# Optimization experiments

Measured on AMD Instinct MI355X. Metric: run time of the kernel, lower is better.

## Reference

```python
import jax, jax.numpy as jnp
import numpy as np

BATCH = 32768
HIDDEN = 512
OUT = 2
FUTURE_STEPS = 60


def _lstm_cell(x, h, c, w_ih, w_hh, b_ih, b_hh):
    # PyTorch gate order: i, f, g, o
    g = x @ w_ih.T + h @ w_hh.T + b_ih + b_hh
    i, f, gg, o = jnp.split(g, 4, axis=-1)
    c_new = jax.nn.sigmoid(f) * c + jax.nn.sigmoid(i) * jnp.tanh(gg)
    h_new = jax.nn.sigmoid(o) * jnp.tanh(c_new)
    return h_new, c_new


def setup_inputs() -> dict:
    key = jax.random.key(0)
    ks = jax.random.split(key, 16)
    s = 0.05
    inp = {
        "h": jax.random.normal(ks[0], (BATCH, HIDDEN), jnp.float32),
        "w_init_h": jax.random.normal(ks[1], (HIDDEN, HIDDEN), jnp.float32) * s,
        "b_init_h": jax.random.normal(ks[2], (HIDDEN,), jnp.float32) * s,
        "w_init_c": jax.random.normal(ks[3], (HIDDEN, HIDDEN), jnp.float32) * s,
        "b_init_c": jax.random.normal(ks[4], (HIDDEN,), jnp.float32) * s,
        "w_ih0": jax.random.normal(ks[5], (4 * HIDDEN, OUT), jnp.float32) * s,
        "w_hh0": jax.random.normal(ks[6], (4 * HIDDEN, HIDDEN), jnp.float32) * s,
        "b_ih0": jax.random.normal(ks[7], (4 * HIDDEN,), jnp.float32) * s,
        "b_hh0": jax.random.normal(ks[8], (4 * HIDDEN,), jnp.float32) * s,
        "w_ih1": jax.random.normal(ks[9], (4 * HIDDEN, HIDDEN), jnp.float32) * s,
        "w_hh1": jax.random.normal(ks[10], (4 * HIDDEN, HIDDEN), jnp.float32) * s,
        "b_ih1": jax.random.normal(ks[11], (4 * HIDDEN,), jnp.float32) * s,
        "b_hh1": jax.random.normal(ks[12], (4 * HIDDEN,), jnp.float32) * s,
        "w_out": jax.random.normal(ks[13], (OUT, HIDDEN), jnp.float32) * s,
        "b_out": jax.random.normal(ks[14], (OUT,), jnp.float32) * s,
    }
    return inp


def reference(h, w_init_h, b_init_h, w_init_c, b_init_c,
              w_ih0, w_hh0, b_ih0, b_hh0,
              w_ih1, w_hh1, b_ih1, b_hh1,
              w_out, b_out):
    batch = h.shape[0]
    # same initial (h, c) replicated to both LSTM layers (repeat(2,1,1))
    h0 = h @ w_init_h.T + b_init_h
    c0 = h @ w_init_c.T + b_init_c
    x0 = jnp.zeros((batch, OUT), h.dtype)

    def step(carry, _):
        x, h1, c1, h2, c2 = carry
        h1, c1 = _lstm_cell(x, h1, c1, w_ih0, w_hh0, b_ih0, b_hh0)
        h2, c2 = _lstm_cell(h1, h2, c2, w_ih1, w_hh1, b_ih1, b_hh1)
        pred = h2 @ w_out.T + b_out  # [batch, OUT]
        return (pred, h1, c1, h2, c2), pred

    _, preds = jax.lax.scan(step, (x0, h0, c0, h0, c0), None, length=FUTURE_STEPS)
    return jnp.transpose(preds, (1, 0, 2))  # [batch, future_steps, OUT]
```

## Files before the change

kernel.cpp:

```cpp
#include <hip/hip_runtime.h>

#define HID    512
#define TPB    512
#define NSTEP  60
#define BMI    64

using f32x4 = __attribute__((ext_vector_type(4))) float;
using s16x8 = __attribute__((ext_vector_type(8))) short;

__device__ __forceinline__ unsigned short f2bf(float f) {
    unsigned u = __builtin_bit_cast(unsigned, f);
    u += 0x7fffu + ((u >> 16) & 1u);
    return (unsigned short)(u >> 16);
}
__device__ __forceinline__ float bf2f(unsigned u) {
    return __builtin_bit_cast(float, u << 16);
}
__device__ __forceinline__ float sigm(float x) { return 1.0f / (1.0f + __expf(-x)); }
__device__ __forceinline__ float tanh_(float x) { return 1.0f - 2.0f / (__expf(2.0f * x) + 1.0f); }

__device__ __forceinline__ f32x4 deperm(f32x4 q, int lgr) {
    f32x4 p;
    if (lgr == 0)      { p[0]=q[0]; p[1]=q[1]; p[2]=q[2]; p[3]=q[3]; }
    else if (lgr == 1) { p[0]=q[1]; p[1]=q[0]; p[2]=q[3]; p[3]=q[2]; }
    else if (lgr == 2) { p[0]=q[2]; p[1]=q[3]; p[2]=q[0]; p[3]=q[1]; }
    else               { p[0]=q[3]; p[1]=q[2]; p[2]=q[1]; p[3]=q[0]; }
    return p;
}

__global__ void pack_kernel(const float* __restrict__ w_hh0, const float* __restrict__ w_ih1,
                            const float* __restrict__ w_hh1, const float* __restrict__ w_init_h,
                            const float* __restrict__ w_init_c,
                            const float* __restrict__ b_ih0, const float* __restrict__ b_hh0,
                            const float* __restrict__ b_ih1, const float* __restrict__ b_hh1,
                            unsigned short* __restrict__ PW1, unsigned short* __restrict__ PW2,
                            unsigned short* __restrict__ PI,
                            float* __restrict__ b1, float* __restrict__ b2)
{
    int idx = blockIdx.x * 256 + threadIdx.x;
    if (idx < 1048576) {
        int el = idx & 511, fr = idx >> 9;
        int ks = fr & 15, ct = (fr >> 4) & 7, s = fr >> 7;
        int lane = el >> 3, e = el & 7;
        int cl = ct * 16 + (lane & 15);
        int gcol = (cl >> 5) * 512 + s * 32 + (cl & 31);
        int k = ks * 32 + (lane >> 4) * 8 + e;
        PW1[idx] = f2bf(w_hh0[gcol * 512 + k]);
        return;
    }
    int i2 = idx - 1048576;
    if (i2 >= 0 && i2 < 2097152) {
        int el = i2 & 511, fr = i2 >> 9;
        int ks = fr & 31, ct = (fr >> 5) & 7, s = fr >> 8;
        int lane = el >> 3, e = el & 7;
        int cl = ct * 16 + (lane & 15);
        int gcol = (cl >> 5) * 512 + s * 32 + (cl & 31);
        int kk = (ks & 15) * 32 + (lane >> 4) * 8 + e;
        float v = (ks < 16) ? w_ih1[gcol * 512 + kk] : w_hh1[gcol * 512 + kk];
        PW2[i2] = f2bf(v);
        return;
    }
    int i3 = idx - (1048576 + 2097152);
    if (i3 >= 0 && i3 < 524288) {
        int el = i3 & 511, fr = i3 >> 9;
        int ks = fr & 15, tile = fr >> 4;
        int s = tile >> 5, c = tile & 31;
        int lane = el >> 3, e = el & 7;
        int n = c * 16 + (lane & 15);
        int k = ks * 32 + (lane >> 4) * 8 + e;
        float v = s ? w_init_c[n * 512 + k] : w_init_h[n * 512 + k];
        PI[i3] = f2bf(v);
        return;
    }
    int i4 = idx - (1048576 + 2097152 + 524288);
    if (i4 >= 0 && i4 < 2048) b1[i4] = b_ih0[i4] + b_hh0[i4];
    else if (i4 >= 2048 && i4 < 4096) b2[i4 - 2048] = b_ih1[i4 - 2048] + b_hh1[i4 - 2048];
}

__global__ __launch_bounds__(TPB, 2) void init_kernel(
    const float* __restrict__ hin, const unsigned short* __restrict__ PI,
    const float* __restrict__ b_init_h, const float* __restrict__ b_init_c,
    unsigned short* __restrict__ h1s, unsigned short* __restrict__ h2s,
    unsigned short* __restrict__ c1s, unsigned short* __restrict__ c2s)
{
    __shared__ unsigned short bufA[BMI * HID];
    const int tid = threadIdx.x, lane = tid & 63, wave = tid >> 6;
    const int m0 = blockIdx.x * BMI;
    const int l15 = lane & 15, lg = lane >> 4;
    const int swz = (lane & 7) << 4;

    for (int j = 0; j < 16; ++j) {
        int e = tid * 4 + j * 2048;
        int row = e >> 9, col = e & 511;
        float4 v = *(const float4*)(hin + (size_t)(m0 + row) * HID + col);
        ushort4 w;
        w.x = f2bf(v.x); w.y = f2bf(v.y); w.z = f2bf(v.z); w.w = f2bf(v.w);
        int L = (row * 1024 + col * 2) ^ ((row & 7) << 4);
        *(ushort4*)((char*)bufA + L) = w;
    }
    __syncthreads();

    #pragma unroll 1
    for (int cc = 0; cc < 4; ++cc) {
        int c = wave * 4 + cc;
        int nc = c * 16 + l15;
        f32x4 acc[4][2];
        #pragma unroll
        for (int rt = 0; rt < 4; ++rt)
            #pragma unroll
            for (int s = 0; s < 2; ++s)
                #pragma unroll
                for (int r = 0; r < 4; ++r) acc[rt][s][r] = 0.0f;

        #pragma unroll
        for (int ks = 0; ks < 16; ++ks) {
            s16x8 a[4];
            #pragma unroll
            for (int rt = 0; rt < 4; ++rt) {
                int ao = (rt * 16 + l15) * 1024 + ((ks * 64 + lg * 16) ^ swz);
                a[rt] = *(const s16x8*)((const char*)bufA + ao);
            }
            #pragma unroll
            for (int s = 0; s < 2; ++s) {
                s16x8 b = ((const s16x8*)PI)[((s * 32 + c) * 16 + ks) * 64 + lane];
                #pragma unroll
                for (int rt = 0; rt < 4; ++rt)
                    acc[rt][s] = __builtin_amdgcn_mfma_f32_16x16x32_bf16(a[rt], b, acc[rt][s], 0, 0, 0);
            }
        }
        float bh = b_init_h[nc], bc = b_init_c[nc];
        #pragma unroll
        for (int rt = 0; rt < 4; ++rt)
            #pragma unroll
            for (int r = 0; r < 4; ++r) {
                int m = m0 + rt * 16 + lg * 4 + r;
                float hv = acc[rt][0][r] + bh;
                float cv = acc[rt][1][r] + bc;
                unsigned short hb = f2bf(hv);
                size_t o = (size_t)m * HID + nc;
                h1s[o] = hb; h2s[o] = hb;
                c1s[o] = f2bf(cv); c2s[o] = f2bf(cv);
            }
    }
}

__global__ __launch_bounds__(TPB, 2) void l1_kernel(
    const unsigned short* __restrict__ h1R, unsigned short* __restrict__ h1W,
    unsigned short* __restrict__ c1s, const float* __restrict__ pp,
    float* __restrict__ outp, const unsigned short* __restrict__ PW1,
    const float* __restrict__ b1, const float* __restrict__ w_ih0,
    const float* __restrict__ b_out, int t)
{
    __shared__ __align__(16) unsigned short Ab[16384];
    __shared__ __align__(16) float gl[2][2][2048];
    __shared__ __align__(16) float xls[5120];

    const int tid = threadIdx.x, lane = tid & 63, w = tid >> 6;
    const int b = blockIdx.x;
    const int g = 2 * (b & 7) + (b >> 7);
    const int s = (b >> 3) & 15;
    const int m0 = g * 2048;
    const int l15 = lane & 15, lg = lane >> 4;
    const int cg = w & 1, kh = (w >> 1) & 1, rha = w >> 2;

    s16x8 bw[4][8];
    #pragma unroll
    for (int j = 0; j < 4; ++j)
        #pragma unroll
        for (int ksl = 0; ksl < 8; ++ksl)
            bw[j][ksl] = ((const s16x8*)PW1)[(((s * 8 + cg * 4 + j) * 16) + kh * 8 + ksl) * 64 + lane];

    const int erow = tid >> 4, ejp = tid & 15;
    const int lgr = w & 3;
    float b1v[8], wiA[8], wiB[8];
    #pragma unroll
    for (int q = 0; q < 8; ++q) {
        int dj = q & 1, gq = q >> 1;
        int gcol = gq * 512 + s * 32 + ejp * 2 + dj;
        b1v[q] = b1[gcol];
        wiA[q] = w_ih0[gcol * 2 + 0];
        wiB[q] = w_ih0[gcol * 2 + 1];
    }
    float bo0 = b_out[0], bo1 = b_out[1];

    if (t == 0) {
        #pragma unroll
        for (int i = 0; i < 8; ++i) xls[tid * 8 + i] = 0.0f;
    } else {
        f32x4 s0 = {0.f,0.f,0.f,0.f}, s1 = {0.f,0.f,0.f,0.f};
        #pragma unroll 1
        for (int ss = 0; ss < 16; ++ss) {
            const float* p = pp + (((size_t)(g * 16 + ss)) << 12) + tid * 8;
            s0 += *(const f32x4*)p;
            s1 += *(const f32x4*)(p + 4);
        }
        s0[0] += bo0; s0[1] += bo1; s0[2] += bo0; s0[3] += bo1;
        s1[0] += bo0; s1[1] += bo1; s1[2] += bo0; s1[3] += bo1;
        *(f32x4*)(xls + tid * 8) = s0;
        *(f32x4*)(xls + tid * 8 + 4) = s1;
        if (s == 0) {
            float* ob = outp + (size_t)(m0 + tid * 4) * (2 * NSTEP) + (t - 1) * 2;
            *(float2*)(ob)                 = make_float2(s0[0], s0[1]);
            *(float2*)(ob + 2 * NSTEP)     = make_float2(s0[2], s0[3]);
            *(float2*)(ob + 4 * NSTEP)     = make_float2(s1[0], s1[1]);
            *(float2*)(ob + 6 * NSTEP)     = make_float2(s1[2], s1[3]);
        }
    }

    const int st_l15 = tid & 15, st_lg = (tid >> 4) & 3, st_rh = (tid >> 6) & 1, st_kq = tid >> 7;
    const int st_grow = st_rh * 16 + st_l15;

    uint4 nv[4];
    #pragma unroll
    for (int p = 0; p < 4; ++p) {
        int ks = p * 4 + st_kq;
        nv[p] = *(const uint4*)(h1R + (size_t)(m0 + st_grow) * HID + ks * 32 + st_lg * 8);
    }
    #pragma unroll
    for (int p = 0; p < 4; ++p)
        *(uint4*)((char*)Ab + p * 8192 + tid * 16) = nv[p];

    #pragma unroll 1
    for (int ch = 0; ch < 64; ++ch) {
        __syncthreads();

        if (ch < 63) {
            #pragma unroll
            for (int p = 0; p < 4; ++p) {
                int ks = p * 4 + st_kq;
                nv[p] = *(const uint4*)(h1R + (size_t)(m0 + (ch + 1) * 32 + st_grow) * HID + ks * 32 + st_lg * 8);
            }
        }

        f32x4 acc[4];
        #pragma unroll
        for (int j = 0; j < 4; ++j) { acc[j][0]=0.f; acc[j][1]=0.f; acc[j][2]=0.f; acc[j][3]=0.f; }
        #pragma unroll
        for (int ksl = 0; ksl < 8; ++ksl) {
            int ks = kh * 8 + ksl;
            s16x8 a = *(const s16x8*)((const char*)Ab + ks * 2048 + rha * 1024 + lane * 16);
            #pragma unroll
            for (int j = 0; j < 4; ++j)
                acc[j] = __builtin_amdgcn_mfma_f32_16x16x32_bf16(a, bw[j][ksl], acc[j], 0, 0, 0);
        }
        #pragma unroll
        for (int j = 0; j < 4; ++j) {
            int col = (cg * 4 + j) * 16 + l15;
            int u = col & 31, gate = col >> 5;
            float* dst = &gl[kh][u & 1][(u >> 1) * 4 + (gate ^ lg)];
            #pragma unroll
            for (int r = 0; r < 4; ++r)
                dst[(rha * 16 + lg * 4 + r) * 64] = acc[j][r];
        }
        __syncthreads();

        if (ch < 63) {
            #pragma unroll
            for (int p = 0; p < 4; ++p)
                *(uint4*)((char*)Ab + p * 8192 + tid * 16) = nv[p];
        }

        {
            int grow = ch * 32 + erow;
            int m = m0 + grow;
            float x0 = xls[grow * 2 + 0], x1 = xls[grow * 2 + 1];
            int gbase = erow * 64 + ejp * 4;
            f32x4 qa = *(const f32x4*)&gl[0][0][gbase];
            qa += *(const f32x4*)&gl[1][0][gbase];
            f32x4 qb = *(const f32x4*)&gl[0][1][gbase];
            qb += *(const f32x4*)&gl[1][1][gbase];
            qa = deperm(qa, lgr); qb = deperm(qb, lgr);

            int cix = m * HID + s * 32 + ejp * 2;
            unsigned cp = *(const unsigned*)(c1s + cix);
            float cold0 = bf2f(cp & 0xffffu), cold1 = bf2f(cp >> 16);
            float i0 = sigm(qa[0] + b1v[0] + x0 * wiA[0] + x1 * wiB[0]);
            float f0 = sigm(qa[1] + b1v[2] + x0 * wiA[2] + x1 * wiB[2]);
            float g0 = tanh_(qa[2] + b1v[4] + x0 * wiA[4] + x1 * wiB[4]);
            float o0 = sigm(qa[3] + b1v[6] + x0 * wiA[6] + x1 * wiB[6]);
            float cn0 = f0 * cold0 + i0 * g0;
            float hn0 = o0 * tanh_(cn0);
            float i1 = sigm(qb[0] + b1v[1] + x0 * wiA[1] + x1 * wiB[1]);
            float f1 = sigm(qb[1] + b1v[3] + x0 * wiA[3] + x1 * wiB[3]);
            float g1 = tanh_(qb[2] + b1v[5] + x0 * wiA[5] + x1 * wiB[5]);
            float o1 = sigm(qb[3] + b1v[7] + x0 * wiA[7] + x1 * wiB[7]);
            float cn1 = f1 * cold1 + i1 * g1;
            float hn1 = o1 * tanh_(cn1);
            __builtin_nontemporal_store((unsigned)f2bf(cn0) | ((unsigned)f2bf(cn1) << 16),
                                        (unsigned*)(c1s + cix));
            __builtin_nontemporal_store((unsigned)f2bf(hn0) | ((unsigned)f2bf(hn1) << 16),
                                        (unsigned*)(h1W + cix));
        }
    }
}

__global__ __launch_bounds__(TPB, 2) void l2_kernel(
    const unsigned short* __restrict__ h1C, const unsigned short* __restrict__ h2R,
    unsigned short* __restrict__ h2W, unsigned short* __restrict__ c2s,
    float* __restrict__ pp,
    const unsigned short* __restrict__ PW2, const float* __restrict__ b2,
    const float* __restrict__ w_out)
{
    __shared__ __align__(16) unsigned short Ab[32768];
    __shared__ __align__(16) float gl[2][2][2304];

    const int tid = threadIdx.x, lane = tid & 63, w = tid >> 6;
    const int b = blockIdx.x;
    const int g = 2 * (b & 7) + (b >> 7);
    const int s = (b >> 3) & 15;
    const int m0 = g * 2048;
    const int l15 = lane & 15, lg = lane >> 4;
    const int cg = w & 1, kq = w >> 1;
    const int copy = kq >> 1, adder = ((kq & 1) == 0);

    s16x8 bw[4][8];
    #pragma unroll
    for (int j = 0; j < 4; ++j)
        #pragma unroll
        for (int ksl = 0; ksl < 8; ++ksl)
            bw[j][ksl] = ((const s16x8*)PW2)[(((s * 8 + cg * 4 + j) * 32) + kq * 8 + ksl) * 64 + lane];

    const int erow = tid >> 4, ejp = tid & 15;
    const int lgr = w & 3;
    float b2v[8];
    #pragma unroll
    for (int q = 0; q < 8; ++q) {
        int dj = q & 1, gq = q >> 1;
        b2v[q] = b2[gq * 512 + s * 32 + ejp * 2 + dj];
    }
    float woA0 = w_out[s * 32 + ejp * 2], woA1 = w_out[s * 32 + ejp * 2 + 1];
    float woB0 = w_out[512 + s * 32 + ejp * 2], woB1 = w_out[512 + s * 32 + ejp * 2 + 1];

    const int st_l15 = tid & 15, st_lg = (tid >> 4) & 3, st_rh = (tid >> 6) & 1, st_kq = tid >> 7;
    const int st_grow = st_rh * 16 + st_l15;

    uint4 nv[8];
    #pragma unroll
    for (int p = 0; p < 8; ++p) {
        int ks = p * 4 + st_kq;
        const unsigned short* src = (ks < 16) ? h1C : h2R;
        int kel = (ks < 16) ? ks : (ks - 16);
        nv[p] = *(const uint4*)(src + (size_t)(m0 + st_grow) * HID + kel * 32 + st_lg * 8);
    }
    #pragma unroll
    for (int p = 0; p < 8; ++p)
        *(uint4*)((char*)Ab + p * 8192 + tid * 16) = nv[p];

    #pragma unroll 1
    for (int ch = 0; ch < 64; ++ch) {
        __syncthreads();

        if (ch < 63) {
            #pragma unroll
            for (int p = 0; p < 8; ++p) {
                int ks = p * 4 + st_kq;
                const unsigned short* src = (ks < 16) ? h1C : h2R;
                int kel = (ks < 16) ? ks : (ks - 16);
                nv[p] = *(const uint4*)(src + (size_t)(m0 + (ch + 1) * 32 + st_grow) * HID + kel * 32 + st_lg * 8);
            }
        }

        f32x4 acc[2][4];
        #pragma unroll
        for (int rh = 0; rh < 2; ++rh)
            #pragma unroll
            for (int j = 0; j < 4; ++j) { acc[rh][j][0]=0.f; acc[rh][j][1]=0.f; acc[rh][j][2]=0.f; acc[rh][j][3]=0.f; }
        #pragma unroll
        for (int ksl = 0; ksl < 8; ++ksl) {
            int ks = kq * 8 + ksl;
            s16x8 a0 = *(const s16x8*)((const char*)Ab + ks * 2048 + lane * 16);
            s16x8 a1 = *(const s16x8*)((const char*)Ab + ks * 2048 + 1024 + lane * 16);
            #pragma unroll
            for (int j = 0; j < 4; ++j) {
                acc[0][j] = __builtin_amdgcn_mfma_f32_16x16x32_bf16(a0, bw[j][ksl], acc[0][j], 0, 0, 0);
                acc[1][j] = __builtin_amdgcn_mfma_f32_16x16x32_bf16(a1, bw[j][ksl], acc[1][j], 0, 0, 0);
            }
        }

        if (!adder) {
            #pragma unroll
            for (int j = 0; j < 4; ++j) {
                int col = (cg * 4 + j) * 16 + l15;
                int u = col & 31, gate = col >> 5;
                float* dst = &gl[copy][u & 1][(u >> 1) * 4 + (gate ^ lg)];
                #pragma unroll
                for (int rh = 0; rh < 2; ++rh)
                    #pragma unroll
                    for (int r = 0; r < 4; ++r)
                        dst[(rh * 16 + lg * 4 + r) * 64] = acc[rh][j][r];
            }
        }
        __syncthreads();
        if (adder) {
            #pragma unroll
            for (int j = 0; j < 4; ++j) {
                int col = (cg * 4 + j) * 16 + l15;
                int u = col & 31, gate = col >> 5;
                float* dst = &gl[copy][u & 1][(u >> 1) * 4 + (gate ^ lg)];
                #pragma unroll
                for (int rh = 0; rh < 2; ++rh)
                    #pragma unroll
                    for (int r = 0; r < 4; ++r)
                        dst[(rh * 16 + lg * 4 + r) * 64] += acc[rh][j][r];
            }
        }
        __syncthreads();

        if (ch < 63) {
            #pragma unroll
            for (int p = 0; p < 8; ++p)
                *(uint4*)((char*)Ab + p * 8192 + tid * 16) = nv[p];
        }

        {
            int m = m0 + ch * 32 + erow;
            int gbase = erow * 64 + ejp * 4;
            f32x4 qa = *(const f32x4*)&gl[0][0][gbase];
            qa += *(const f32x4*)&gl[1][0][gbase];
            f32x4 qb = *(const f32x4*)&gl[0][1][gbase];
            qb += *(const f32x4*)&gl[1][1][gbase];
            qa = deperm(qa, lgr); qb = deperm(qb, lgr);

            int cix = m * HID + s * 32 + ejp * 2;
            unsigned cp = *(const unsigned*)(c2s + cix);
            float cold0 = bf2f(cp & 0xffffu), cold1 = bf2f(cp >> 16);
            float i0 = sigm(qa[0] + b2v[0]);
            float f0 = sigm(qa[1] + b2v[2]);
            float g0 = tanh_(qa[2] + b2v[4]);
            float o0 = sigm(qa[3] + b2v[6]);
            float cn0 = f0 * cold0 + i0 * g0;
            float hn0 = o0 * tanh_(cn0);
            float i1 = sigm(qb[0] + b2v[1]);
            float f1 = sigm(qb[1] + b2v[3]);
            float g1 = tanh_(qb[2] + b2v[5]);
            float o1 = sigm(qb[3] + b2v[7]);
            float cn1 = f1 * cold1 + i1 * g1;
            float hn1 = o1 * tanh_(cn1);
            __builtin_nontemporal_store((unsigned)f2bf(cn0) | ((unsigned)f2bf(cn1) << 16),
                                        (unsigned*)(c2s + cix));
            __builtin_nontemporal_store((unsigned)f2bf(hn0) | ((unsigned)f2bf(hn1) << 16),
                                        (unsigned*)(h2W + cix));

            float p0 = hn0 * woA0 + hn1 * woA1;
            float p1 = hn0 * woB0 + hn1 * woB1;
            #pragma unroll
            for (int d = 1; d < 16; d <<= 1) {
                p0 += __shfl_xor(p0, d, 16);
                p1 += __shfl_xor(p1, d, 16);
            }
            if (ejp == 0)
                *(float2*)(pp + (((size_t)(g * 16 + s)) << 12) + (size_t)(ch * 32 + erow) * 2)
                    = make_float2(p0, p1);
        }
    }
}

__global__ void tail_kernel(const float* __restrict__ pp, const float* __restrict__ b_out,
                            float* __restrict__ outp)
{
    int i = blockIdx.x * 256 + threadIdx.x;
    if (i < 65536) {
        int m = i >> 1, j = i & 1;
        int g = m >> 11;
        int idx = (m & 2047) * 2 + j;
        float sum = b_out[j];
        #pragma unroll 1
        for (int s = 0; s < 16; ++s)
            sum += pp[(((size_t)(g * 16 + s)) << 12) + idx];
        outp[(size_t)m * (2 * NSTEP) + (NSTEP - 1) * 2 + j] = sum;
    }
}

extern "C" void kernel_launch(void* const* d_in, const int* in_sizes, int n_in,
                              void* d_out, int out_size, void* d_ws, size_t ws_size,
                              hipStream_t stream)
{
    (void)in_sizes; (void)n_in; (void)out_size; (void)ws_size;
    const float* h        = (const float*)d_in[0];
    const float* w_init_h = (const float*)d_in[1];
    const float* b_init_h = (const float*)d_in[2];
    const float* w_init_c = (const float*)d_in[3];
    const float* b_init_c = (const float*)d_in[4];
    const float* w_ih0    = (const float*)d_in[5];
    const float* w_hh0    = (const float*)d_in[6];
    const float* b_ih0    = (const float*)d_in[7];
    const float* b_hh0    = (const float*)d_in[8];
    const float* w_ih1    = (const float*)d_in[9];
    const float* w_hh1    = (const float*)d_in[10];
    const float* b_ih1    = (const float*)d_in[11];
    const float* b_hh1    = (const float*)d_in[12];
    const float* w_out    = (const float*)d_in[13];
    const float* b_out    = (const float*)d_in[14];
    float* out = (float*)d_out;

    char* ws = (char*)d_ws;
    unsigned short* h1s[2] = { (unsigned short*)(ws + 0),
                               (unsigned short*)(ws + 33554432) };
    unsigned short* h2s[2] = { (unsigned short*)(ws + 67108864),
                               (unsigned short*)(ws + 100663296) };
    unsigned short* c1s = (unsigned short*)(ws + 134217728);
    unsigned short* c2s = (unsigned short*)(ws + 167772160);
    float* pp           = (float*)(ws + 201326592);
    unsigned short* PW1 = (unsigned short*)(ws + 205520896);
    unsigned short* PW2 = (unsigned short*)(ws + 207618048);
    unsigned short* PI  = (unsigned short*)(ws + 211812352);
    float* b1 = (float*)(ws + 212860928);
    float* b2 = (float*)(ws + 212869120);

    pack_kernel<<<14352, 256, 0, stream>>>(w_hh0, w_ih1, w_hh1, w_init_h, w_init_c,
                                           b_ih0, b_hh0, b_ih1, b_hh1, PW1, PW2, PI, b1, b2);
    init_kernel<<<32768 / BMI, TPB, 0, stream>>>(h, PI, b_init_h, b_init_c,
                                                 h1s[1], h2s[1], c1s, c2s);
    for (int t = 0; t < NSTEP; ++t) {
        const unsigned short* h1R = h1s[(t + 1) & 1];
        unsigned short* h1W = h1s[t & 1];
        const unsigned short* h2R = h2s[(t + 1) & 1];
        unsigned short* h2W = h2s[t & 1];
        l1_kernel<<<256, TPB, 0, stream>>>(h1R, h1W, c1s, pp, out, PW1, b1, w_ih0, b_out, t);
        l2_kernel<<<256, TPB, 0, stream>>>(h1W, h2R, h2W, c2s, pp, PW2, b2, w_out);
    }
    tail_kernel<<<256, 256, 0, stream>>>(pp, b_out, out);
}
```

Baseline: 41.11 ms.

## Reorder packed weight columns and restructure LSTM step kernels' pipeline and gate reduction

```diff
diff --git a/kernel.cpp b/kernel.cpp
--- a/kernel.cpp
+++ b/kernel.cpp
@@ -18,15 +18,6 @@
 }
 __device__ __forceinline__ float sigm(float x) { return 1.0f / (1.0f + __expf(-x)); }
 __device__ __forceinline__ float tanh_(float x) { return 1.0f - 2.0f / (__expf(2.0f * x) + 1.0f); }
-
-__device__ __forceinline__ f32x4 deperm(f32x4 q, int lgr) {
-    f32x4 p;
-    if (lgr == 0)      { p[0]=q[0]; p[1]=q[1]; p[2]=q[2]; p[3]=q[3]; }
-    else if (lgr == 1) { p[0]=q[1]; p[1]=q[0]; p[2]=q[3]; p[3]=q[2]; }
-    else if (lgr == 2) { p[0]=q[2]; p[1]=q[3]; p[2]=q[0]; p[3]=q[1]; }
-    else               { p[0]=q[3]; p[1]=q[2]; p[2]=q[1]; p[3]=q[0]; }
-    return p;
-}
 
 __global__ void pack_kernel(const float* __restrict__ w_hh0, const float* __restrict__ w_ih1,
                             const float* __restrict__ w_hh1, const float* __restrict__ w_init_h,
@@ -42,8 +33,8 @@
         int el = idx & 511, fr = idx >> 9;
         int ks = fr & 15, ct = (fr >> 4) & 7, s = fr >> 7;
         int lane = el >> 3, e = el & 7;
-        int cl = ct * 16 + (lane & 15);
-        int gcol = (cl >> 5) * 512 + s * 32 + (cl & 31);
+        int l15 = lane & 15;
+        int gcol = (l15 & 3) * 512 + s * 32 + ct * 4 + (l15 >> 2);
         int k = ks * 32 + (lane >> 4) * 8 + e;
         PW1[idx] = f2bf(w_hh0[gcol * 512 + k]);
         return;
@@ -53,8 +44,8 @@
         int el = i2 & 511, fr = i2 >> 9;
         int ks = fr & 31, ct = (fr >> 5) & 7, s = fr >> 8;
         int lane = el >> 3, e = el & 7;
-        int cl = ct * 16 + (lane & 15);
-        int gcol = (cl >> 5) * 512 + s * 32 + (cl & 31);
+        int l15 = lane & 15;
+        int gcol = (l15 & 3) * 512 + s * 32 + ct * 4 + (l15 >> 2);
         int kk = (ks & 15) * 32 + (lane >> 4) * 8 + e;
         float v = (ks < 16) ? w_ih1[gcol * 512 + kk] : w_hh1[gcol * 512 + kk];
         PW2[i2] = f2bf(v);
@@ -152,8 +143,8 @@
     const float* __restrict__ b_out, int t)
 {
     __shared__ __align__(16) unsigned short Ab[16384];
-    __shared__ __align__(16) float gl[2][2][2048];
-    __shared__ __align__(16) float xls[5120];
+    __shared__ __align__(16) float glf[2 * 4224];
+    __shared__ __align__(16) float xls[4096];
 
     const int tid = threadIdx.x, lane = tid & 63, w = tid >> 6;
     const int b = blockIdx.x;
@@ -161,17 +152,16 @@
     const int s = (b >> 3) & 15;
     const int m0 = g * 2048;
     const int l15 = lane & 15, lg = lane >> 4;
-    const int cg = w & 1, kh = (w >> 1) & 1, rha = w >> 2;
-
-    s16x8 bw[4][8];
-    #pragma unroll
-    for (int j = 0; j < 4; ++j)
+    const int cg = w >> 1, kh = w & 1;
+
+    s16x8 bw[2][8];
+    #pragma unroll
+    for (int j = 0; j < 2; ++j)
         #pragma unroll
         for (int ksl = 0; ksl < 8; ++ksl)
-            bw[j][ksl] = ((const s16x8*)PW1)[(((s * 8 + cg * 4 + j) * 16) + kh * 8 + ksl) * 64 + lane];
+            bw[j][ksl] = ((const s16x8*)PW1)[(((s * 8 + cg * 2 + j) * 16) + kh * 8 + ksl) * 64 + lane];
 
     const int erow = tid >> 4, ejp = tid & 15;
-    const int lgr = w & 3;
     float b1v[8], wiA[8], wiB[8];
     #pragma unroll
     for (int q = 0; q < 8; ++q) {
@@ -200,10 +190,10 @@
         *(f32x4*)(xls + tid * 8 + 4) = s1;
         if (s == 0) {
             float* ob = outp + (size_t)(m0 + tid * 4) * (2 * NSTEP) + (t - 1) * 2;
-            *(float2*)(ob)                 = make_float2(s0[0], s0[1]);
-            *(float2*)(ob + 2 * NSTEP)     = make_float2(s0[2], s0[3]);
-            *(float2*)(ob + 4 * NSTEP)     = make_float2(s1[0], s1[1]);
-            *(float2*)(ob + 6 * NSTEP)     = make_float2(s1[2], s1[3]);
+            *(float2*)(ob)             = make_float2(s0[0], s0[1]);
+            *(float2*)(ob + 2 * NSTEP) = make_float2(s0[2], s0[3]);
+            *(float2*)(ob + 4 * NSTEP) = make_float2(s1[0], s1[1]);
+            *(float2*)(ob + 6 * NSTEP) = make_float2(s1[2], s1[3]);
         }
     }
 
@@ -214,66 +204,73 @@
     #pragma unroll
     for (int p = 0; p < 4; ++p) {
         int ks = p * 4 + st_kq;
-        nv[p] = *(const uint4*)(h1R + (size_t)(m0 + st_grow) * HID + ks * 32 + st_lg * 8);
-    }
-    #pragma unroll
-    for (int p = 0; p < 4; ++p)
-        *(uint4*)((char*)Ab + p * 8192 + tid * 16) = nv[p];
+        uint4 v = *(const uint4*)(h1R + (size_t)(m0 + st_grow) * HID + ks * 32 + st_lg * 8);
+        *(uint4*)((char*)Ab + p * 8192 + tid * 16) = v;
+    }
+    #pragma unroll
+    for (int p = 0; p < 4; ++p) {
+        int ks = p * 4 + st_kq;
+        nv[p] = *(const uint4*)(h1R + (size_t)(m0 + 32 + st_grow) * HID + ks * 32 + st_lg * 8);
+    }
+    unsigned cpr = *(const unsigned*)(c1s + (size_t)(m0 + erow) * HID + s * 32 + ejp * 2);
+    __syncthreads();
 
     #pragma unroll 1
     for (int ch = 0; ch < 64; ++ch) {
+        f32x4 acc[2][2];
+        #pragma unroll
+        for (int j = 0; j < 2; ++j)
+            #pragma unroll
+            for (int rh = 0; rh < 2; ++rh) { acc[j][rh][0]=0.f; acc[j][rh][1]=0.f; acc[j][rh][2]=0.f; acc[j][rh][3]=0.f; }
+        #pragma unroll
+        for (int ksl = 0; ksl < 8; ++ksl) {
+            int ks = kh * 8 + ksl;
+            s16x8 a0 = *(const s16x8*)((const char*)Ab + ks * 2048 + lane * 16);
+            s16x8 a1 = *(const s16x8*)((const char*)Ab + ks * 2048 + 1024 + lane * 16);
+            #pragma unroll
+            for (int j = 0; j < 2; ++j) {
+                acc[j][0] = __builtin_amdgcn_mfma_f32_16x16x32_bf16(a0, bw[j][ksl], acc[j][0], 0, 0, 0);
+                acc[j][1] = __builtin_amdgcn_mfma_f32_16x16x32_bf16(a1, bw[j][ksl], acc[j][1], 0, 0, 0);
+            }
+        }
+        #pragma unroll
+        for (int j = 0; j < 2; ++j) {
+            int col = (cg * 2 + j) * 16 + l15;
+            #pragma unroll
+            for (int rh = 0; rh < 2; ++rh)
+                #pragma unroll
+                for (int r = 0; r < 4; ++r)
+                    glf[kh * 4224 + (rh * 16 + lg * 4 + r) * 132 + col] = acc[j][rh][r];
+        }
         __syncthreads();
 
         if (ch < 63) {
+            #pragma unroll
+            for (int p = 0; p < 4; ++p)
+                *(uint4*)((char*)Ab + p * 8192 + tid * 16) = nv[p];
+        }
+        if (ch < 62) {
             #pragma unroll
             for (int p = 0; p < 4; ++p) {
                 int ks = p * 4 + st_kq;
-                nv[p] = *(const uint4*)(h1R + (size_t)(m0 + (ch + 1) * 32 + st_grow) * HID + ks * 32 + st_lg * 8);
-            }
-        }
-
-        f32x4 acc[4];
-        #pragma unroll
-        for (int j = 0; j < 4; ++j) { acc[j][0]=0.f; acc[j][1]=0.f; acc[j][2]=0.f; acc[j][3]=0.f; }
-        #pragma unroll
-        for (int ksl = 0; ksl < 8; ++ksl) {
-            int ks = kh * 8 + ksl;
-            s16x8 a = *(const s16x8*)((const char*)Ab + ks * 2048 + rha * 1024 + lane * 16);
-            #pragma unroll
-            for (int j = 0; j < 4; ++j)
-                acc[j] = __builtin_amdgcn_mfma_f32_16x16x32_bf16(a, bw[j][ksl], acc[j], 0, 0, 0);
-        }
-        #pragma unroll
-        for (int j = 0; j < 4; ++j) {
-            int col = (cg * 4 + j) * 16 + l15;
-            int u = col & 31, gate = col >> 5;
-            float* dst = &gl[kh][u & 1][(u >> 1) * 4 + (gate ^ lg)];
-            #pragma unroll
-            for (int r = 0; r < 4; ++r)
-                dst[(rha * 16 + lg * 4 + r) * 64] = acc[j][r];
-        }
-        __syncthreads();
-
-        if (ch < 63) {
-            #pragma unroll
-            for (int p = 0; p < 4; ++p)
-                *(uint4*)((char*)Ab + p * 8192 + tid * 16) = nv[p];
-        }
+                nv[p] = *(const uint4*)(h1R + (size_t)(m0 + (ch + 2) * 32 + st_grow) * HID + ks * 32 + st_lg * 8);
+            }
+        }
+        unsigned cnx = 0;
+        if (ch < 63)
+            cnx = *(const unsigned*)(c1s + (size_t)(m0 + (ch + 1) * 32 + erow) * HID + s * 32 + ejp * 2);
 
         {
             int grow = ch * 32 + erow;
             int m = m0 + grow;
             float x0 = xls[grow * 2 + 0], x1 = xls[grow * 2 + 1];
-            int gbase = erow * 64 + ejp * 4;
-            f32x4 qa = *(const f32x4*)&gl[0][0][gbase];
-            qa += *(const f32x4*)&gl[1][0][gbase];
-            f32x4 qb = *(const f32x4*)&gl[0][1][gbase];
-            qb += *(const f32x4*)&gl[1][1][gbase];
-            qa = deperm(qa, lgr); qb = deperm(qb, lgr);
-
-            int cix = m * HID + s * 32 + ejp * 2;
-            unsigned cp = *(const unsigned*)(c1s + cix);
-            float cold0 = bf2f(cp & 0xffffu), cold1 = bf2f(cp >> 16);
+            int gbase = erow * 132 + ejp * 8;
+            f32x4 qa = *(const f32x4*)&glf[gbase];
+            qa += *(const f32x4*)&glf[4224 + gbase];
+            f32x4 qb = *(const f32x4*)&glf[gbase + 4];
+            qb += *(const f32x4*)&glf[4224 + gbase + 4];
+
+            float cold0 = bf2f(cpr & 0xffffu), cold1 = bf2f(cpr >> 16);
             float i0 = sigm(qa[0] + b1v[0] + x0 * wiA[0] + x1 * wiB[0]);
             float f0 = sigm(qa[1] + b1v[2] + x0 * wiA[2] + x1 * wiB[2]);
             float g0 = tanh_(qa[2] + b1v[4] + x0 * wiA[4] + x1 * wiB[4]);
@@ -286,11 +283,12 @@
             float o1 = sigm(qb[3] + b1v[7] + x0 * wiA[7] + x1 * wiB[7]);
             float cn1 = f1 * cold1 + i1 * g1;
             float hn1 = o1 * tanh_(cn1);
-            __builtin_nontemporal_store((unsigned)f2bf(cn0) | ((unsigned)f2bf(cn1) << 16),
-                                        (unsigned*)(c1s + cix));
-            __builtin_nontemporal_store((unsigned)f2bf(hn0) | ((unsigned)f2bf(hn1) << 16),
-                                        (unsigned*)(h1W + cix));
-        }
+            size_t cix = (size_t)m * HID + s * 32 + ejp * 2;
+            *(unsigned*)(c1s + cix) = (unsigned)f2bf(cn0) | ((unsigned)f2bf(cn1) << 16);
+            *(unsigned*)(h1W + cix) = (unsigned)f2bf(hn0) | ((unsigned)f2bf(hn1) << 16);
+        }
+        cpr = cnx;
+        __syncthreads();
     }
 }
 
@@ -302,7 +300,7 @@
     const float* __restrict__ w_out)
 {
     __shared__ __align__(16) unsigned short Ab[32768];
-    __shared__ __align__(16) float gl[2][2][2304];
+    __shared__ __align__(16) float glf[2 * 4224];
 
     const int tid = threadIdx.x, lane = tid & 63, w = tid >> 6;
     const int b = blockIdx.x;
@@ -310,18 +308,16 @@
     const int s = (b >> 3) & 15;
     const int m0 = g * 2048;
     const int l15 = lane & 15, lg = lane >> 4;
-    const int cg = w & 1, kq = w >> 1;
-    const int copy = kq >> 1, adder = ((kq & 1) == 0);
-
-    s16x8 bw[4][8];
-    #pragma unroll
-    for (int j = 0; j < 4; ++j)
-        #pragma unroll
-        for (int ksl = 0; ksl < 8; ++ksl)
-            bw[j][ksl] = ((const s16x8*)PW2)[(((s * 8 + cg * 4 + j) * 32) + kq * 8 + ksl) * 64 + lane];
+    const int cg = w >> 1, kh = w & 1;
+
+    s16x8 bw[2][16];
+    #pragma unroll
+    for (int j = 0; j < 2; ++j)
+        #pragma unroll
+        for (int ksl = 0; ksl < 16; ++ksl)
+            bw[j][ksl] = ((const s16x8*)PW2)[(((s * 8 + cg * 2 + j) * 32) + kh * 16 + ksl) * 64 + lane];
 
     const int erow = tid >> 4, ejp = tid & 15;
-    const int lgr = w & 3;
     float b2v[8];
     #pragma unroll
     for (int q = 0; q < 8; ++q) {
@@ -340,90 +336,76 @@
         int ks = p * 4 + st_kq;
         const unsigned short* src = (ks < 16) ? h1C : h2R;
         int kel = (ks < 16) ? ks : (ks - 16);
-        nv[p] = *(const uint4*)(src + (size_t)(m0 + st_grow) * HID + kel * 32 + st_lg * 8);
-    }
-    #pragma unroll
-    for (int p = 0; p < 8; ++p)
-        *(uint4*)((char*)Ab + p * 8192 + tid * 16) = nv[p];
+        uint4 v = *(const uint4*)(src + (size_t)(m0 + st_grow) * HID + kel * 32 + st_lg * 8);
+        *(uint4*)((char*)Ab + p * 8192 + tid * 16) = v;
+    }
+    #pragma unroll
+    for (int p = 0; p < 8; ++p) {
+        int ks = p * 4 + st_kq;
+        const unsigned short* src = (ks < 16) ? h1C : h2R;
+        int kel = (ks < 16) ? ks : (ks - 16);
+        nv[p] = *(const uint4*)(src + (size_t)(m0 + 32 + st_grow) * HID + kel * 32 + st_lg * 8);
+    }
+    unsigned cpr = *(const unsigned*)(c2s + (size_t)(m0 + erow) * HID + s * 32 + ejp * 2);
+    __syncthreads();
 
     #pragma unroll 1
     for (int ch = 0; ch < 64; ++ch) {
+        f32x4 acc[2][2];
+        #pragma unroll
+        for (int j = 0; j < 2; ++j)
+            #pragma unroll
+            for (int rh = 0; rh < 2; ++rh) { acc[j][rh][0]=0.f; acc[j][rh][1]=0.f; acc[j][rh][2]=0.f; acc[j][rh][3]=0.f; }
+        #pragma unroll
+        for (int ksl = 0; ksl < 16; ++ksl) {
+            int ks = kh * 16 + ksl;
+            s16x8 a0 = *(const s16x8*)((const char*)Ab + ks * 2048 + lane * 16);
+            s16x8 a1 = *(const s16x8*)((const char*)Ab + ks * 2048 + 1024 + lane * 16);
+            #pragma unroll
+            for (int j = 0; j < 2; ++j) {
+                acc[j][0] = __builtin_amdgcn_mfma_f32_16x16x32_bf16(a0, bw[j][ksl], acc[j][0], 0, 0, 0);
+                acc[j][1] = __builtin_amdgcn_mfma_f32_16x16x32_bf16(a1, bw[j][ksl], acc[j][1], 0, 0, 0);
+            }
+        }
+        #pragma unroll
+        for (int j = 0; j < 2; ++j) {
+            int col = (cg * 2 + j) * 16 + l15;
+            #pragma unroll
+            for (int rh = 0; rh < 2; ++rh)
+                #pragma unroll
+                for (int r = 0; r < 4; ++r)
+                    glf[kh * 4224 + (rh * 16 + lg * 4 + r) * 132 + col] = acc[j][rh][r];
+        }
         __syncthreads();
 
         if (ch < 63) {
+            #pragma unroll
+            for (int p = 0; p < 8; ++p)
+                *(uint4*)((char*)Ab + p * 8192 + tid * 16) = nv[p];
+        }
+        if (ch < 62) {
             #pragma unroll
             for (int p = 0; p < 8; ++p) {
                 int ks = p * 4 + st_kq;
                 const unsigned short* src = (ks < 16) ? h1C : h2R;
                 int kel = (ks < 16) ? ks : (ks - 16);
-                nv[p] = *(const uint4*)(src + (size_t)(m0 + (ch + 1) * 32 + st_grow) * HID + kel * 32 + st_lg * 8);
-            }
-        }
-
-        f32x4 acc[2][4];
-        #pragma unroll
-        for (int rh = 0; rh < 2; ++rh)
-            #pragma unroll
-            for (int j = 0; j < 4; ++j) { acc[rh][j][0]=0.f; acc[rh][j][1]=0.f; acc[rh][j][2]=0.f; acc[rh][j][3]=0.f; }
-        #pragma unroll
-        for (int ksl = 0; ksl < 8; ++ksl) {
-            int ks = kq * 8 + ksl;
-            s16x8 a0 = *(const s16x8*)((const char*)Ab + ks * 2048 + lane * 16);
-            s16x8 a1 = *(const s16x8*)((const char*)Ab + ks * 2048 + 1024 + lane * 16);
-            #pragma unroll
-            for (int j = 0; j < 4; ++j) {
-                acc[0][j] = __builtin_amdgcn_mfma_f32_16x16x32_bf16(a0, bw[j][ksl], acc[0][j], 0, 0, 0);
-                acc[1][j] = __builtin_amdgcn_mfma_f32_16x16x32_bf16(a1, bw[j][ksl], acc[1][j], 0, 0, 0);
-            }
-        }
-
-        if (!adder) {
-            #pragma unroll
-            for (int j = 0; j < 4; ++j) {
-                int col = (cg * 4 + j) * 16 + l15;
-                int u = col & 31, gate = col >> 5;
-                float* dst = &gl[copy][u & 1][(u >> 1) * 4 + (gate ^ lg)];
-                #pragma unroll
-                for (int rh = 0; rh < 2; ++rh)
-                    #pragma unroll
-                    for (int r = 0; r < 4; ++r)
-                        dst[(rh * 16 + lg * 4 + r) * 64] = acc[rh][j][r];
-            }
-        }
-        __syncthreads();
-        if (adder) {
-            #pragma unroll
-            for (int j = 0; j < 4; ++j) {
-                int col = (cg * 4 + j) * 16 + l15;
-                int u = col & 31, gate = col >> 5;
-                float* dst = &gl[copy][u & 1][(u >> 1) * 4 + (gate ^ lg)];
-                #pragma unroll
-                for (int rh = 0; rh < 2; ++rh)
-                    #pragma unroll
-                    for (int r = 0; r < 4; ++r)
-                        dst[(rh * 16 + lg * 4 + r) * 64] += acc[rh][j][r];
-            }
-        }
-        __syncthreads();
-
-        if (ch < 63) {
-            #pragma unroll
-            for (int p = 0; p < 8; ++p)
-                *(uint4*)((char*)Ab + p * 8192 + tid * 16) = nv[p];
-        }
+                nv[p] = *(const uint4*)(src + (size_t)(m0 + (ch + 2) * 32 + st_grow) * HID + kel * 32 + st_lg * 8);
+            }
+        }
+        unsigned cnx = 0;
+        if (ch < 63)
+            cnx = *(const unsigned*)(c2s + (size_t)(m0 + (ch + 1) * 32 + erow) * HID + s * 32 + ejp * 2);
 
         {
-            int m = m0 + ch * 32 + erow;
-            int gbase = erow * 64 + ejp * 4;
-            f32x4 qa = *(const f32x4*)&gl[0][0][gbase];
-            qa += *(const f32x4*)&gl[1][0][gbase];
-            f32x4 qb = *(const f32x4*)&gl[0][1][gbase];
-            qb += *(const f32x4*)&gl[1][1][gbase];
-            qa = deperm(qa, lgr); qb = deperm(qb, lgr);
-
-            int cix = m * HID + s * 32 + ejp * 2;
-            unsigned cp = *(const unsigned*)(c2s + cix);
-            float cold0 = bf2f(cp & 0xffffu), cold1 = bf2f(cp >> 16);
+            int grow = ch * 32 + erow;
+            int m = m0 + grow;
+            int gbase = erow * 132 + ejp * 8;
+            f32x4 qa = *(const f32x4*)&glf[gbase];
+            qa += *(const f32x4*)&glf[4224 + gbase];
+            f32x4 qb = *(const f32x4*)&glf[gbase + 4];
+            qb += *(const f32x4*)&glf[4224 + gbase + 4];
+
+            float cold0 = bf2f(cpr & 0xffffu), cold1 = bf2f(cpr >> 16);
             float i0 = sigm(qa[0] + b2v[0]);
             float f0 = sigm(qa[1] + b2v[2]);
             float g0 = tanh_(qa[2] + b2v[4]);
@@ -436,10 +418,9 @@
             float o1 = sigm(qb[3] + b2v[7]);
             float cn1 = f1 * cold1 + i1 * g1;
             float hn1 = o1 * tanh_(cn1);
-            __builtin_nontemporal_store((unsigned)f2bf(cn0) | ((unsigned)f2bf(cn1) << 16),
-                                        (unsigned*)(c2s + cix));
-            __builtin_nontemporal_store((unsigned)f2bf(hn0) | ((unsigned)f2bf(hn1) << 16),
-                                        (unsigned*)(h2W + cix));
+            size_t cix = (size_t)m * HID + s * 32 + ejp * 2;
+            *(unsigned*)(c2s + cix) = (unsigned)f2bf(cn0) | ((unsigned)f2bf(cn1) << 16);
+            *(unsigned*)(h2W + cix) = (unsigned)f2bf(hn0) | ((unsigned)f2bf(hn1) << 16);
 
             float p0 = hn0 * woA0 + hn1 * woA1;
             float p1 = hn0 * woB0 + hn1 * woB1;
@@ -449,9 +430,11 @@
                 p1 += __shfl_xor(p1, d, 16);
             }
             if (ejp == 0)
-                *(float2*)(pp + (((size_t)(g * 16 + s)) << 12) + (size_t)(ch * 32 + erow) * 2)
+                *(float2*)(pp + (((size_t)(g * 16 + s)) << 12) + (size_t)grow * 2)
                     = make_float2(p0, p1);
         }
+        cpr = cnx;
+        __syncthreads();
     }
 }
 
```

Result: faster. 37.85 ms (-7.9%).
